# Performance work log

Hardware: AMD Instinct MI355X
Metric: run time of the kernel (lower is better)

Reference implementation:

```python
import jax, jax.numpy as jnp
import numpy as np
from jax import lax

B, C, H, W = 8, 128, 128, 128


def setup_inputs() -> dict:
    key = jax.random.key(0)
    ks = jax.random.split(key, 10)
    s = 0.02
    return {
        "x": jax.random.normal(ks[0], (B, C, H, W), jnp.float32),
        "ln_w": jnp.ones((C,), jnp.float32),
        "ln_b": jnp.zeros((C,), jnp.float32),
        "qkv_w": jax.random.normal(ks[1], (3 * C, C, 1, 1), jnp.float32) * s,
        "qkv_b": jnp.zeros((3 * C,), jnp.float32),
        "dw_w": jax.random.normal(ks[2], (3 * C, 1, 3, 3), jnp.float32) * s,
        "dw_b": jnp.zeros((3 * C,), jnp.float32),
        "proj_w": jax.random.normal(ks[3], (C, C, 1, 1), jnp.float32) * s,
        "proj_b": jnp.zeros((C,), jnp.float32),
        "temp1": jnp.ones((1, 1), jnp.float32),
        "temp2": jnp.ones((1, 1), jnp.float32),
    }


def reference(x, ln_w, ln_b, qkv_w, qkv_b, dw_w, dw_b, proj_w, proj_b, temp1, temp2):
    Cd = x.shape[1]

    def ln(t):  # WithBias LayerNorm over channel dim (unbiased=False var)
        mu = t.mean(axis=1, keepdims=True)
        var = ((t - mu) ** 2).mean(axis=1, keepdims=True)
        return (t - mu) / jnp.sqrt(var + 1e-5) * ln_w[None, :, None, None] + ln_b[None, :, None, None]

    def conv1(t, w, b):  # 1x1 conv
        return jnp.einsum('bchw,oc->bohw', t, w[:, :, 0, 0]) + b[None, :, None, None]

    def dwc(t):  # depthwise 3x3, pad 1
        y = lax.conv_general_dilated(t, dw_w, (1, 1), ((1, 1), (1, 1)),
                                     dimension_numbers=('NCHW', 'OIHW', 'NCHW'),
                                     feature_group_count=t.shape[1])
        return y + dw_b[None, :, None, None]

    def l2n(t):  # F.normalize over last axis, eps=1e-12
        return t / jnp.maximum(jnp.linalg.norm(t, axis=-1, keepdims=True), 1e-12)

    # ---- stage 1: pool over H, attention over W (channel-pooled) ----
    qkv = dwc(conv1(ln(x), qkv_w, qkv_b))
    q1, k1, v1 = qkv[:, :Cd], qkv[:, Cd:2 * Cd], qkv[:, 2 * Cd:]
    q1 = l2n(q1.mean(axis=2)[:, None])           # [B,1,C,W]
    k1 = l2n(k1.max(axis=2)[:, None])            # [B,1,C,W]
    attn1 = jax.nn.softmax(jnp.einsum('bocw,bocv->bowv', q1, k1) * temp1, axis=-1)  # [B,1,W,W]
    out1 = jnp.einsum('bchw,bowv->bchv', v1, attn1)
    out1 = x + conv1(out1, proj_w, proj_b)

    # ---- stage 2: pool over C, attention over H ----
    qkv = dwc(conv1(ln(out1), qkv_w, qkv_b))
    q2, k2, v2 = qkv[:, :Cd], qkv[:, Cd:2 * Cd], qkv[:, 2 * Cd:]
    q2 = l2n(q2.mean(axis=1)[:, None])           # [B,1,H,W]
    k2 = l2n(k2.mean(axis=1)[:, None])           # [B,1,H,W]
    attn2 = jax.nn.softmax(jnp.einsum('bohw,bogw->bohg', q2, k2) * temp2, axis=-1)  # [B,1,H,H]
    out2 = jnp.einsum('bchw,bohg->bcgw', v2, attn2)  # = (v^T @ attn)^T
    out = conv1(out2, proj_w, proj_b) + out1
    return out
```

## Files before the change

kernel.cpp:

```cpp
#include <hip/hip_runtime.h>

typedef __attribute__((ext_vector_type(8))) short bf16x8;
typedef __attribute__((ext_vector_type(4))) float f32x4;
typedef __attribute__((ext_vector_type(4))) unsigned short us4;
typedef __attribute__((ext_vector_type(4))) unsigned int u32x4;

static constexpr int CC = 128, NN = 16384;
static constexpr int O3 = 384;
static constexpr long long CN  = (long long)CC * NN;
static constexpr long long O3N = (long long)O3 * NN;

__device__ __forceinline__ float wave_sum(float v) {
  for (int o = 32; o; o >>= 1) v += __shfl_xor(v, o);
  return v;
}
__device__ __forceinline__ float wave_max(float v) {
  for (int o = 32; o; o >>= 1) v = fmaxf(v, __shfl_xor(v, o));
  return v;
}
__device__ __forceinline__ unsigned short f2bf(float f) {
  unsigned u = __float_as_uint(f);
  u += 0x7FFF + ((u >> 16) & 1);
  return (unsigned short)(u >> 16);
}
__device__ __forceinline__ float bf2f(unsigned short h) {
  return __uint_as_float((unsigned)h << 16);
}

__global__ __launch_bounds__(64) void k_prep(const float* __restrict__ qkvw,
                                             const float* __restrict__ qkvb,
                                             const float* __restrict__ lnw,
                                             const float* __restrict__ lnb,
                                             const float* __restrict__ projw,
                                             unsigned short* __restrict__ Aq,
                                             unsigned short* __restrict__ Ap,
                                             float* __restrict__ Svec,
                                             float* __restrict__ bias2) {
  int o = blockIdx.x, t = threadIdx.x;
  if (o < O3) {
    float w0 = qkvw[o * 128 + t], w1 = qkvw[o * 128 + t + 64];
    unsigned short h0 = f2bf(w0 * lnw[t]), h1 = f2bf(w1 * lnw[t + 64]);
    Aq[o * 128 + t] = h0; Aq[o * 128 + t + 64] = h1;
    float s = wave_sum(bf2f(h0) + bf2f(h1));
    float bs = wave_sum(w0 * lnb[t] + w1 * lnb[t + 64]);
    if (t == 0) { Svec[o] = s; bias2[o] = qkvb[o] + bs; }
  } else {
    int r = o - O3;
    Ap[r * 128 + t] = f2bf(projw[r * 128 + t]);
    Ap[r * 128 + t + 64] = f2bf(projw[r * 128 + t + 64]);
  }
}

__global__ __launch_bounds__(256) void k_qkv_mfma(
    const void* __restrict__ srcp, const float* __restrict__ mu, const float* __restrict__ rs,
    const unsigned short* __restrict__ Aq, const float* __restrict__ Svec,
    const float* __restrict__ bias2, unsigned short* __restrict__ out,
    int b0, int useg, int srcbf) {
  __shared__ unsigned short As[128 * 136];
  __shared__ unsigned short Bs[64 * 128];
  __shared__ float muL[64], rsL[64];
  int bz = blockIdx.z, bg = b0 + bz;
  int p = blockIdx.x;
  int hi = p / 24, rr0 = p - hi * 24;
  int m0 = (rr0 >> 3) * 128;
  int n0 = (hi * 8 + (rr0 & 7)) * 64;
  int t = threadIdx.x, w = t >> 6, l = t & 63;
  int lr = l & 15, lg = l >> 4;

  {
    const unsigned short* Asrc = Aq + (size_t)m0 * 128;
#pragma unroll
    for (int r = 0; r < 8; ++r) {
      int v = r * 256 + t;
      int m = v >> 4, c8 = (v & 15) * 8;
      *(u32x4*)&As[m * 136 + c8] = *(const u32x4*)&Asrc[m * 128 + c8];
    }
  }
  {
    int n = t & 63, cb = t >> 6;
    if (!srcbf) {
      const float* xb = (const float*)srcp + (size_t)bg * CN + n0;
      float xr[32];
#pragma unroll
      for (int g = 0; g < 4; ++g)
#pragma unroll
        for (int q = 0; q < 8; ++q)
          xr[g * 8 + q] = xb[(size_t)((cb * 4 + g) * 8 + q) * NN + n];
#pragma unroll
      for (int g = 0; g < 4; ++g) {
        int c8 = (cb * 4 + g) * 8;
        unsigned pk[4];
#pragma unroll
        for (int q = 0; q < 4; ++q) {
          unsigned short a = f2bf(xr[g * 8 + 2 * q]);
          unsigned short b = f2bf(xr[g * 8 + 2 * q + 1]);
          pk[q] = (unsigned)a | ((unsigned)b << 16);
        }
        int c8s = c8 ^ ((n & 7) << 3);
        *(u32x4*)&Bs[n * 128 + c8s] = *(const u32x4*)pk;
      }
    } else {
      const unsigned short* xb = (const unsigned short*)srcp + (size_t)bg * CN + n0;
      unsigned short xr[32];
#pragma unroll
      for (int g = 0; g < 4; ++g)
#pragma unroll
        for (int q = 0; q < 8; ++q)
          xr[g * 8 + q] = xb[(size_t)((cb * 4 + g) * 8 + q) * NN + n];
#pragma unroll
      for (int g = 0; g < 4; ++g) {
        int c8 = (cb * 4 + g) * 8;
        unsigned pk[4];
#pragma unroll
        for (int q = 0; q < 4; ++q)
          pk[q] = (unsigned)xr[g * 8 + 2 * q] | ((unsigned)xr[g * 8 + 2 * q + 1] << 16);
        int c8s = c8 ^ ((n & 7) << 3);
        *(u32x4*)&Bs[n * 128 + c8s] = *(const u32x4*)pk;
      }
    }
  }
  __syncthreads();

  if (!useg) {
    int pp = t >> 2, sub = t & 3;
    float s1 = 0.f, s2 = 0.f;
#pragma unroll
    for (int b2 = 0; b2 < 4; ++b2) {
      int c8 = (sub * 4 + b2) * 8;
      int c8s = c8 ^ ((pp & 7) << 3);
      bf16x8 v = *(const bf16x8*)&Bs[pp * 128 + c8s];
#pragma unroll
      for (int q = 0; q < 8; ++q) {
        float f = bf2f((unsigned short)v[q]);
        s1 += f; s2 += f * f;
      }
    }
    s1 += __shfl_xor(s1, 1); s2 += __shfl_xor(s2, 1);
    s1 += __shfl_xor(s1, 2); s2 += __shfl_xor(s2, 2);
    if (sub == 0) {
      float m = s1 * (1.f / 128.f);
      muL[pp] = m;
      rsL[pp] = rsqrtf(s2 * (1.f / 128.f) - m * m + 1e-5f);
    }
    __syncthreads();
  }

  f32x4 acc[2][4];
#pragma unroll
  for (int i = 0; i < 2; ++i)
#pragma unroll
    for (int j = 0; j < 4; ++j) acc[i][j] = (f32x4){0.f, 0.f, 0.f, 0.f};
#pragma unroll
  for (int ks = 0; ks < 4; ++ks) {
    bf16x8 bfr[4];
#pragma unroll
    for (int j = 0; j < 4; ++j) {
      int row = 16 * j + lr;
      int col = (ks * 32 + lg * 8) ^ ((lr & 7) << 3);
      bfr[j] = *(const bf16x8*)&Bs[row * 128 + col];
    }
#pragma unroll
    for (int i = 0; i < 2; ++i) {
      bf16x8 afr = *(const bf16x8*)&As[(32 * w + 16 * i + lr) * 136 + ks * 32 + lg * 8];
#pragma unroll
      for (int j = 0; j < 4; ++j)
        acc[i][j] = __builtin_amdgcn_mfma_f32_16x16x32_bf16(afr, bfr[j], acc[i][j], 0, 0, 0);
    }
  }

  float rsv[4], muv[4];
#pragma unroll
  for (int j = 0; j < 4; ++j) {
    int nl = 16 * j + lr;
    if (useg) {
      rsv[j] = rs[(size_t)bg * NN + n0 + nl];
      muv[j] = mu[(size_t)bg * NN + n0 + nl];
    } else {
      rsv[j] = rsL[nl];
      muv[j] = muL[nl];
    }
  }
  __syncthreads();
  unsigned short* Os = As;
#pragma unroll
  for (int i = 0; i < 2; ++i) {
    int obl = 32 * w + 16 * i + lg * 4;
    float sv[4], bv[4];
#pragma unroll
    for (int r2 = 0; r2 < 4; ++r2) { sv[r2] = Svec[m0 + obl + r2]; bv[r2] = bias2[m0 + obl + r2]; }
#pragma unroll
    for (int j = 0; j < 4; ++j)
#pragma unroll
      for (int r2 = 0; r2 < 4; ++r2)
        Os[(obl + r2) * 72 + 16 * j + lr] =
            f2bf(rsv[j] * (acc[i][j][r2] - muv[j] * sv[r2]) + bv[r2]);
  }
  __syncthreads();
#pragma unroll
  for (int r = 0; r < 4; ++r) {
    int idx = r * 256 + t;
    int row = idx >> 3, ch = idx & 7;
    unsigned short* op = out + (size_t)bz * O3N + (size_t)(m0 + row) * NN + n0 + ch * 8;
    *(u32x4*)op = *(const u32x4*)&Os[row * 72 + ch * 8];
  }
}

__global__ __launch_bounds__(1024) void k_dwc(unsigned short* __restrict__ buf,
                                              const float* __restrict__ dww,
                                              const float* __restrict__ dwb,
                                              float* __restrict__ qm,
                                              float* __restrict__ km,
                                              int b0, int stage) {
  __shared__ unsigned short pl[130 * 144];
  __shared__ float red[32 * 128];
  int o = blockIdx.x, bz = blockIdx.y, bg = b0 + bz;
  int t = threadIdx.x;
  unsigned short* base = buf + (size_t)bz * O3N + (size_t)o * NN;
  unsigned* pl32 = (unsigned*)pl;

  for (int i = t; i < 1168; i += 1024) {
    int idx;
    if (i < 72) idx = i;
    else if (i < 144) idx = 129 * 72 + (i - 72);
    else { int j = i - 144; int row = (j >> 3) + 1; int s = j & 7;
           idx = row * 72 + (s < 4 ? s : 64 + s); }
    pl32[idx] = 0u;
  }
  __syncthreads();
#pragma unroll
  for (int r = 0; r < 2; ++r) {
    int idx = r * 1024 + t;
    int row = idx >> 4, c8 = (idx & 15) * 8;
    *(u32x4*)&pl[(row + 1) * 144 + 8 + c8] = *(const u32x4*)&base[row * 128 + c8];
  }
  __syncthreads();

  const float* wg = dww + o * 9;
  float w00 = wg[0], w01 = wg[1], w02 = wg[2];
  float w10 = wg[3], w11 = wg[4], w12 = wg[5];
  float w20 = wg[6], w21 = wg[7], w22 = wg[8];
  float bias = dwb[o];
  int mode = (stage == 0) ? (o < 128 ? 1 : (o < 256 ? 2 : 0)) : 0;
  int hh0 = t >> 5, w0 = (t & 31) * 4;
  float csum[4] = {0.f, 0.f, 0.f, 0.f};
  float cmax[4] = {-1e30f, -1e30f, -1e30f, -1e30f};

#pragma unroll
  for (int g = 0; g < 4; ++g) {
    int h = g * 32 + hh0;
    float a0 = bias, a1 = bias, a2 = bias, a3 = bias;
#pragma unroll
    for (int dr = 0; dr < 3; ++dr) {
      const unsigned short* rp = &pl[(h + dr) * 144];
      us4 cA = *(const us4*)&rp[w0 + 4];
      us4 cB = *(const us4*)&rp[w0 + 8];
      us4 cC = *(const us4*)&rp[w0 + 12];
      float f0 = bf2f(cA[3]), f1 = bf2f(cB[0]), f2 = bf2f(cB[1]);
      float f3 = bf2f(cB[2]), f4 = bf2f(cB[3]), f5 = bf2f(cC[0]);
      float wr0 = (dr == 0) ? w00 : (dr == 1 ? w10 : w20);
      float wr1 = (dr == 0) ? w01 : (dr == 1 ? w11 : w21);
      float wr2 = (dr == 0) ? w02 : (dr == 1 ? w12 : w22);
      a0 += f0 * wr0 + f1 * wr1 + f2 * wr2;
      a1 += f1 * wr0 + f2 * wr1 + f3 * wr2;
      a2 += f2 * wr0 + f3 * wr1 + f4 * wr2;
      a3 += f3 * wr0 + f4 * wr1 + f5 * wr2;
    }
    if (mode == 0) {
      us4 ov;
      ov[0] = f2bf(a0); ov[1] = f2bf(a1); ov[2] = f2bf(a2); ov[3] = f2bf(a3);
      *(us4*)&base[g * 4096 + t * 4] = ov;
    } else if (mode == 1) {
      csum[0] += a0; csum[1] += a1; csum[2] += a2; csum[3] += a3;
    } else {
      cmax[0] = fmaxf(cmax[0], a0); cmax[1] = fmaxf(cmax[1], a1);
      cmax[2] = fmaxf(cmax[2], a2); cmax[3] = fmaxf(cmax[3], a3);
    }
  }

  if (mode) {
    int j = t >> 5;
#pragma unroll
    for (int dx = 0; dx < 4; ++dx)
      red[j * 128 + w0 + dx] = (mode == 1) ? csum[dx] : cmax[dx];
    __syncthreads();
    if (t < 128) {
      float v = red[t];
      if (mode == 1) {
        for (int jj = 1; jj < 32; ++jj) v += red[jj * 128 + t];
        qm[(size_t)bg * NN + o * 128 + t] = v * (1.f / 128.f);
      } else {
        for (int jj = 1; jj < 32; ++jj) v = fmaxf(v, red[jj * 128 + t]);
        km[(size_t)bg * NN + (o - 128) * 128 + t] = v;
      }
    }
  }
}

__global__ __launch_bounds__(256) void k_reduce2(const unsigned short* __restrict__ qkv,
                                                 float* __restrict__ qm, float* __restrict__ km,
                                                 int b0) {
  int bz = blockIdx.y;
  int n = blockIdx.x * 256 + threadIdx.x;
  const unsigned short* base = qkv + (size_t)bz * O3N + n;
  float sq = 0.f, sk = 0.f;
#pragma unroll 4
  for (int c = 0; c < 128; ++c) {
    sq += bf2f(base[(size_t)c * NN]);
    sk += bf2f(base[(size_t)(c + 128) * NN]);
  }
  size_t off = (size_t)(b0 + bz) * NN + n;
  qm[off] = sq * (1.f / 128.f);
  km[off] = sk * (1.f / 128.f);
}

__global__ void k_norm2(float* __restrict__ qm, float* __restrict__ km, int row0) {
  float* buf = blockIdx.y ? km : qm;
  int r = row0 + blockIdx.x, t = threadIdx.x;
  float* p = buf + (size_t)r * 128;
  float v0 = p[t], v1 = p[t + 64];
  float s = wave_sum(v0 * v0 + v1 * v1);
  float sc = 1.f / fmaxf(sqrtf(s), 1e-12f);
  p[t] = v0 * sc;
  p[t + 64] = v1 * sc;
}

__global__ void k_attn1(const float* __restrict__ qm, const float* __restrict__ km,
                        const float* __restrict__ temp, unsigned short* __restrict__ attnT,
                        int b0) {
  int bg = b0 + blockIdx.y;
  int i = blockIdx.x, t = threadIdx.x;
  const float* qb = qm + (size_t)bg * NN;
  const float* kb = km + (size_t)bg * NN;
  __shared__ float qcol[128];
  __shared__ float wred[2];
  qcol[t] = qb[t * 128 + i];
  __syncthreads();
  float s = 0.f;
#pragma unroll 4
  for (int k = 0; k < 128; ++k) s += qcol[k] * kb[k * 128 + t];
  s *= temp[0];
  int wid = t >> 6, lane = t & 63;
  float mx = wave_max(s);
  if (lane == 0) wred[wid] = mx;
  __syncthreads();
  mx = fmaxf(wred[0], wred[1]);
  float pv = __expf(s - mx);
  __syncthreads();
  float sm = wave_sum(pv);
  if (lane == 0) wred[wid] = sm;
  __syncthreads();
  float denom = wred[0] + wred[1];
  attnT[(size_t)bg * NN + (size_t)t * 128 + i] = f2bf(pv / denom);
}

__global__ void k_attn2(const float* __restrict__ qm, const float* __restrict__ km,
                        const float* __restrict__ temp, unsigned short* __restrict__ attnT,
                        int b0) {
  int bg = b0 + blockIdx.y;
  int i = blockIdx.x, t = threadIdx.x;
  const float* qb = qm + (size_t)bg * NN + i * 128;
  const float* kb = km + (size_t)bg * NN + (size_t)t * 128;
  __shared__ float qrow[128];
  __shared__ float wred[2];
  qrow[t] = qb[t];
  __syncthreads();
  float s = 0.f;
#pragma unroll 4
  for (int w = 0; w < 128; ++w) s += qrow[w] * kb[w];
  s *= temp[0];
  int wid = t >> 6, lane = t & 63;
  float mx = wave_max(s);
  if (lane == 0) wred[wid] = mx;
  __syncthreads();
  mx = fmaxf(wred[0], wred[1]);
  float pv = __expf(s - mx);
  __syncthreads();
  float sm = wave_sum(pv);
  if (lane == 0) wred[wid] = sm;
  __syncthreads();
  float denom = wred[0] + wred[1];
  attnT[(size_t)bg * NN + (size_t)t * 128 + i] = f2bf(pv / denom);
}

__global__ __launch_bounds__(256) void k_ap1(const unsigned short* __restrict__ buf,
                                             const unsigned short* __restrict__ attnT,
                                             const unsigned short* __restrict__ Ap,
                                             const float* __restrict__ pb,
                                             const float* __restrict__ x,
                                             unsigned short* __restrict__ out1,
                                             float* __restrict__ mu, float* __restrict__ rs,
                                             int b0) {
  __shared__ __attribute__((aligned(16))) unsigned short S[32768];
  unsigned short* TA = S;
  unsigned short* TB = S + 16384;
  int h = blockIdx.x, bz = blockIdx.z, bg = b0 + bz;
  int t = threadIdx.x, wv = t >> 6, l = t & 63, lr = l & 15, lg = l >> 4;

  {
    const unsigned short* vbase = buf + (size_t)bz * O3N + (size_t)256 * NN;
    const unsigned short* abase = attnT + (size_t)bg * NN;
#pragma unroll
    for (int r = 0; r < 8; ++r) {
      int idx = r * 256 + t;
      int row = idx >> 4, c8 = (idx & 15) * 8;
      int c8s = c8 ^ ((row & 7) << 3);
      *(u32x4*)&TA[row * 128 + c8s] = *(const u32x4*)&vbase[((size_t)row * 128 + h) * 128 + c8];
      *(u32x4*)&TB[row * 128 + c8s] = *(const u32x4*)&abase[row * 128 + c8];
    }
  }
  __syncthreads();

  f32x4 acc[2][8];
#pragma unroll
  for (int i = 0; i < 2; ++i)
#pragma unroll
    for (int j = 0; j < 8; ++j) acc[i][j] = (f32x4){0.f, 0.f, 0.f, 0.f};
#pragma unroll
  for (int ks = 0; ks < 4; ++ks) {
    int colx = (ks * 32 + lg * 8) ^ ((lr & 7) << 3);
    bf16x8 bfr[8];
#pragma unroll
    for (int j = 0; j < 8; ++j)
      bfr[j] = *(const bf16x8*)&TB[(16 * j + lr) * 128 + colx];
#pragma unroll
    for (int i = 0; i < 2; ++i) {
      bf16x8 afr = *(const bf16x8*)&TA[(32 * wv + 16 * i + lr) * 128 + colx];
#pragma unroll
      for (int j = 0; j < 8; ++j)
        acc[i][j] = __builtin_amdgcn_mfma_f32_16x16x32_bf16(afr, bfr[j], acc[i][j], 0, 0, 0);
    }
  }
  __syncthreads();

#pragma unroll
  for (int i = 0; i < 2; ++i) {
    int c0 = 32 * wv + 16 * i + lg * 4;
#pragma unroll
    for (int j = 0; j < 8; ++j) {
      int v = 16 * j + lr;
      us4 ov;
#pragma unroll
      for (int r2 = 0; r2 < 4; ++r2) ov[r2] = f2bf(acc[i][j][r2]);
      *(us4*)&TA[v * 128 + (c0 ^ ((v & 7) << 3))] = ov;
    }
  }
#pragma unroll
  for (int r = 0; r < 8; ++r) {
    int idx = r * 256 + t;
    int row = idx >> 4, c8 = (idx & 15) * 8;
    *(u32x4*)&TB[row * 128 + (c8 ^ ((row & 7) << 3))] = *(const u32x4*)&Ap[row * 128 + c8];
  }
  __syncthreads();

#pragma unroll
  for (int i = 0; i < 2; ++i)
#pragma unroll
    for (int j = 0; j < 8; ++j) acc[i][j] = (f32x4){0.f, 0.f, 0.f, 0.f};
#pragma unroll
  for (int ks = 0; ks < 4; ++ks) {
    int colx = (ks * 32 + lg * 8) ^ ((lr & 7) << 3);
    bf16x8 bfr[8];
#pragma unroll
    for (int j = 0; j < 8; ++j)
      bfr[j] = *(const bf16x8*)&TA[(16 * j + lr) * 128 + colx];
#pragma unroll
    for (int i = 0; i < 2; ++i) {
      bf16x8 afr = *(const bf16x8*)&TB[(32 * wv + 16 * i + lr) * 128 + colx];
#pragma unroll
      for (int j = 0; j < 8; ++j)
        acc[i][j] = __builtin_amdgcn_mfma_f32_16x16x32_bf16(afr, bfr[j], acc[i][j], 0, 0, 0);
    }
  }
  __syncthreads();

  unsigned short* Os = S;
  float* red1 = (float*)(S + 17408);
  float* red2 = red1 + 128 * 17;
  float s1p[8], s2p[8];
#pragma unroll
  for (int j = 0; j < 8; ++j) { s1p[j] = 0.f; s2p[j] = 0.f; }
#pragma unroll
  for (int i = 0; i < 2; ++i) {
    int o0 = 32 * wv + 16 * i + lg * 4;
    float bv[4];
#pragma unroll
    for (int r2 = 0; r2 < 4; ++r2) bv[r2] = pb[o0 + r2];
#pragma unroll
    for (int j = 0; j < 8; ++j) {
      int n = h * 128 + 16 * j + lr;
#pragma unroll
      for (int r2 = 0; r2 < 4; ++r2) {
        size_t off = (size_t)bg * CN + (size_t)(o0 + r2) * NN + n;
        float val = acc[i][j][r2] + bv[r2] + x[off];
        Os[(o0 + r2) * 136 + 16 * j + lr] = f2bf(val);
        s1p[j] += val;
        s2p[j] += val * val;
      }
    }
  }
#pragma unroll
  for (int j = 0; j < 8; ++j) {
    red1[(16 * j + lr) * 17 + (wv * 4 + lg)] = s1p[j];
    red2[(16 * j + lr) * 17 + (wv * 4 + lg)] = s2p[j];
  }
  __syncthreads();
#pragma unroll
  for (int r = 0; r < 8; ++r) {
    int idx = r * 256 + t;
    int row = idx >> 4, ch = idx & 15;
    unsigned short* op = out1 + (size_t)bg * CN + (size_t)row * NN + h * 128 + ch * 8;
    *(u32x4*)op = *(const u32x4*)&Os[row * 136 + ch * 8];
  }
  if (t < 128) {
    float s1 = 0.f, s2 = 0.f;
#pragma unroll
    for (int kk = 0; kk < 16; ++kk) { s1 += red1[t * 17 + kk]; s2 += red2[t * 17 + kk]; }
    float m = s1 * (1.f / 128.f);
    float var = s2 * (1.f / 128.f) - m * m;
    mu[(size_t)bg * NN + h * 128 + t] = m;
    rs[(size_t)bg * NN + h * 128 + t] = rsqrtf(var + 1e-5f);
  }
}

__global__ __launch_bounds__(256) void k_apply2_mfma(unsigned short* __restrict__ buf,
                                                     const unsigned short* __restrict__ attnT,
                                                     int b0) {
  __shared__ unsigned short At[128 * 136];
  __shared__ unsigned short Bt[128 * 136];
  int bz = blockIdx.z, bg = b0 + bz, c = blockIdx.x;
  int t = threadIdx.x, w = t >> 6, l = t & 63, lr = l & 15, lg = l >> 4;
  const unsigned short* vsrc = buf + (size_t)bz * O3N + (size_t)(256 + c) * NN;
  const unsigned short* asrc = attnT + (size_t)bg * NN;
#pragma unroll
  for (int r = 0; r < 8; ++r) {
    int idx = r * 256 + t;
    int row = idx >> 4, c8 = (idx & 15) * 8;
    *(u32x4*)&At[row * 136 + c8] = *(const u32x4*)&asrc[row * 128 + c8];
    us4 lo = *(const us4*)&vsrc[row * 128 + c8];
    us4 hi = *(const us4*)&vsrc[row * 128 + c8 + 4];
#pragma unroll
    for (int q = 0; q < 4; ++q) {
      Bt[(c8 + q) * 136 + row] = lo[q];
      Bt[(c8 + 4 + q) * 136 + row] = hi[q];
    }
  }
  __syncthreads();
  f32x4 acc[2][8];
#pragma unroll
  for (int i = 0; i < 2; ++i)
#pragma unroll
    for (int j = 0; j < 8; ++j) acc[i][j] = (f32x4){0.f, 0.f, 0.f, 0.f};
#pragma unroll
  for (int ks = 0; ks < 4; ++ks) {
    bf16x8 bfr[8];
#pragma unroll
    for (int j = 0; j < 8; ++j)
      bfr[j] = *(const bf16x8*)&Bt[(16 * j + lr) * 136 + ks * 32 + lg * 8];
#pragma unroll
    for (int i = 0; i < 2; ++i) {
      bf16x8 afr = *(const bf16x8*)&At[(32 * w + 16 * i + lr) * 136 + ks * 32 + lg * 8];
#pragma unroll
      for (int j = 0; j < 8; ++j)
        acc[i][j] = __builtin_amdgcn_mfma_f32_16x16x32_bf16(afr, bfr[j], acc[i][j], 0, 0, 0);
    }
  }
  __syncthreads();
  unsigned short* Os = At;
#pragma unroll
  for (int i = 0; i < 2; ++i)
#pragma unroll
    for (int j = 0; j < 8; ++j)
#pragma unroll
      for (int r2 = 0; r2 < 4; ++r2) {
        int g = 32 * w + 16 * i + lg * 4 + r2;
        Os[g * 136 + 16 * j + lr] = f2bf(acc[i][j][r2]);
      }
  __syncthreads();
  unsigned short* ob = buf + (size_t)bz * O3N + (size_t)c * NN;
#pragma unroll
  for (int r = 0; r < 8; ++r) {
    int idx = r * 256 + t;
    int row = idx >> 4, ch = idx & 15;
    *(u32x4*)&ob[(size_t)row * 128 + ch * 8] = *(const u32x4*)&Os[row * 136 + ch * 8];
  }
}

__global__ __launch_bounds__(256) void k_proj_mfma(
    const unsigned short* __restrict__ tin, const unsigned short* __restrict__ Ap,
    const float* __restrict__ pb, const unsigned short* __restrict__ res,
    float* __restrict__ dst, int b0) {
  __shared__ unsigned short Al[128 * 136];
  __shared__ unsigned short Bs2[64 * 128];
  int bz = blockIdx.z, bg = b0 + bz;
  int n0 = blockIdx.x * 64;
  int t = threadIdx.x, w = t >> 6, l = t & 63, lr = l & 15, lg = l >> 4;
  const unsigned short* tb = tin + (size_t)bz * O3N + n0;

#pragma unroll
  for (int r = 0; r < 8; ++r) {
    int v = r * 256 + t;
    int m = v >> 4, c8 = (v & 15) * 8;
    *(u32x4*)&Al[m * 136 + c8] = *(const u32x4*)&Ap[m * 128 + c8];
  }
  {
    int n = t & 63, cb = t >> 6;
    unsigned short vr[32];
#pragma unroll
    for (int g = 0; g < 4; ++g)
#pragma unroll
      for (int q = 0; q < 8; ++q)
        vr[g * 8 + q] = tb[(size_t)((cb * 4 + g) * 8 + q) * NN + n];
#pragma unroll
    for (int g = 0; g < 4; ++g) {
      int c8 = (cb * 4 + g) * 8;
      unsigned pk[4];
#pragma unroll
      for (int q = 0; q < 4; ++q)
        pk[q] = (unsigned)vr[g * 8 + 2 * q] | ((unsigned)vr[g * 8 + 2 * q + 1] << 16);
      int c8s = c8 ^ ((n & 7) << 3);
      *(u32x4*)&Bs2[n * 128 + c8s] = *(const u32x4*)pk;
    }
  }
  __syncthreads();

  f32x4 acc[2][4];
#pragma unroll
  for (int i = 0; i < 2; ++i)
#pragma unroll
    for (int j = 0; j < 4; ++j) acc[i][j] = (f32x4){0.f, 0.f, 0.f, 0.f};

#pragma unroll
  for (int ks = 0; ks < 4; ++ks) {
    bf16x8 bfr[4];
#pragma unroll
    for (int j = 0; j < 4; ++j) {
      int row = 16 * j + lr;
      int col = (ks * 32 + lg * 8) ^ ((lr & 7) << 3);
      bfr[j] = *(const bf16x8*)&Bs2[row * 128 + col];
    }
#pragma unroll
    for (int i = 0; i < 2; ++i) {
      bf16x8 afr = *(const bf16x8*)&Al[(32 * w + 16 * i + lr) * 136 + ks * 32 + lg * 8];
#pragma unroll
      for (int j = 0; j < 4; ++j)
        acc[i][j] = __builtin_amdgcn_mfma_f32_16x16x32_bf16(afr, bfr[j], acc[i][j], 0, 0, 0);
    }
  }

#pragma unroll
  for (int i = 0; i < 2; ++i) {
    int ob = 32 * w + 16 * i + lg * 4;
    float bv[4];
#pragma unroll
    for (int r2 = 0; r2 < 4; ++r2) bv[r2] = pb[ob + r2];
#pragma unroll
    for (int j = 0; j < 4; ++j) {
      int n = n0 + 16 * j + lr;
#pragma unroll
      for (int r2 = 0; r2 < 4; ++r2) {
        size_t off = (size_t)bg * CN + (size_t)(ob + r2) * NN + n;
        dst[off] = acc[i][j][r2] + bv[r2] + bf2f(res[off]);
      }
    }
  }
}

extern "C" void kernel_launch(void* const* d_in, const int* in_sizes, int n_in,
                              void* d_out, int out_size, void* d_ws, size_t ws_size,
                              hipStream_t stream) {
  (void)in_sizes; (void)n_in; (void)out_size;
  const float* x     = (const float*)d_in[0];
  const float* lnw   = (const float*)d_in[1];
  const float* lnb   = (const float*)d_in[2];
  const float* qkvw  = (const float*)d_in[3];
  const float* qkvb  = (const float*)d_in[4];
  const float* dww   = (const float*)d_in[5];
  const float* dwb   = (const float*)d_in[6];
  const float* projw = (const float*)d_in[7];
  const float* projb = (const float*)d_in[8];
  const float* temp1 = (const float*)d_in[9];
  const float* temp2 = (const float*)d_in[10];
  float* out = (float*)d_out;
  float* ws = (float*)d_ws;

  auto needBytes = [&](int nb) {
    return ((size_t)nb * (O3N / 2) + 4ull * CN + 4ull * 131072 + 65536 + 768 + 24576 + 8192) * 4;
  };
  int NB = 8;
  while (NB > 1 && ws_size < needBytes(NB)) NB >>= 1;
  if (ws_size < needBytes(1)) return;

  unsigned short* convbuf = (unsigned short*)ws;
  unsigned short* out1 = (unsigned short*)(ws + (size_t)NB * (O3N / 2));
  float* mu = ws + (size_t)NB * (O3N / 2) + 4ull * CN;
  float* rs = mu + 131072;
  float* qm = rs + 131072;
  float* km = qm + 131072;
  unsigned short* attnT = (unsigned short*)(km + 131072);
  float* Svec  = (float*)(attnT + 8ull * NN);
  float* bias2 = Svec + 384;
  unsigned short* Aq = (unsigned short*)(bias2 + 384);
  unsigned short* Ap = Aq + 49152;

  k_prep<<<512, 64, 0, stream>>>(qkvw, qkvb, lnw, lnb, projw, Aq, Ap, Svec, bias2);

  for (int b0 = 0; b0 < 8; b0 += NB) {
    k_qkv_mfma<<<dim3(768, 1, NB), 256, 0, stream>>>(x, mu, rs, Aq, Svec, bias2, convbuf,
                                                     b0, 0, 0);
    k_dwc<<<dim3(384, NB), 1024, 0, stream>>>(convbuf, dww, dwb, qm, km, b0, 0);
    k_norm2<<<dim3(NB * 128, 2), 64, 0, stream>>>(qm, km, b0 * 128);
    k_attn1<<<dim3(128, NB), 128, 0, stream>>>(qm, km, temp1, attnT, b0);
    k_ap1<<<dim3(128, 1, NB), 256, 0, stream>>>(convbuf, attnT, Ap, projb, x, out1, mu, rs, b0);
  }
  for (int b0 = 0; b0 < 8; b0 += NB) {
    k_qkv_mfma<<<dim3(768, 1, NB), 256, 0, stream>>>(out1, mu, rs, Aq, Svec, bias2, convbuf,
                                                     b0, 1, 1);
    k_dwc<<<dim3(384, NB), 1024, 0, stream>>>(convbuf, dww, dwb, qm, km, b0, 1);
    k_reduce2<<<dim3(64, NB), 256, 0, stream>>>(convbuf, qm, km, b0);
    k_norm2<<<dim3(NB * 128, 2), 64, 0, stream>>>(qm, km, b0 * 128);
    k_attn2<<<dim3(128, NB), 128, 0, stream>>>(qm, km, temp2, attnT, b0);
    k_apply2_mfma<<<dim3(128, 1, NB), 256, 0, stream>>>(convbuf, attnT, b0);
    k_proj_mfma<<<dim3(256, 1, NB), 256, 0, stream>>>(convbuf, Ap, projb, out1, out, b0);
  }
}
```

Baseline: 276.3 us.

## Vectorize B-tile global loads, use packed bf16 conversions, merge syncs

After: 276.8 us. No clear change (+0.2%).

```diff
diff --git a/kernel.cpp b/kernel.cpp
--- a/kernel.cpp
+++ b/kernel.cpp
@@ -1,4 +1,5 @@
 #include <hip/hip_runtime.h>
+#include <hip/hip_bf16.h>
 
 typedef __attribute__((ext_vector_type(8))) short bf16x8;
 typedef __attribute__((ext_vector_type(4))) float f32x4;
@@ -14,14 +15,13 @@
   for (int o = 32; o; o >>= 1) v += __shfl_xor(v, o);
   return v;
 }
-__device__ __forceinline__ float wave_max(float v) {
-  for (int o = 32; o; o >>= 1) v = fmaxf(v, __shfl_xor(v, o));
-  return v;
+__device__ __forceinline__ unsigned pk2bf(float a, float b) {
+  __hip_bfloat162 h = __float22bfloat162_rn(make_float2(a, b));
+  return *reinterpret_cast<unsigned*>(&h);
 }
 __device__ __forceinline__ unsigned short f2bf(float f) {
-  unsigned u = __float_as_uint(f);
-  u += 0x7FFF + ((u >> 16) & 1);
-  return (unsigned short)(u >> 16);
+  __hip_bfloat16 h = __float2bfloat16(f);
+  return *reinterpret_cast<unsigned short*>(&h);
 }
 __device__ __forceinline__ float bf2f(unsigned short h) {
   return __uint_as_float((unsigned)h << 16);
@@ -77,45 +77,37 @@
     }
   }
   {
-    int n = t & 63, cb = t >> 6;
+    int pg = t & 15, cbk = t >> 4;
+    int c8 = cbk * 8;
     if (!srcbf) {
-      const float* xb = (const float*)srcp + (size_t)bg * CN + n0;
-      float xr[32];
-#pragma unroll
-      for (int g = 0; g < 4; ++g)
-#pragma unroll
-        for (int q = 0; q < 8; ++q)
-          xr[g * 8 + q] = xb[(size_t)((cb * 4 + g) * 8 + q) * NN + n];
-#pragma unroll
-      for (int g = 0; g < 4; ++g) {
-        int c8 = (cb * 4 + g) * 8;
+      const float* xb = (const float*)srcp + (size_t)bg * CN + n0 + pg * 4;
+      float4 v[8];
+#pragma unroll
+      for (int ch = 0; ch < 8; ++ch)
+        v[ch] = *(const float4*)&xb[(size_t)(c8 + ch) * NN];
+#pragma unroll
+      for (int pp = 0; pp < 4; ++pp) {
         unsigned pk[4];
 #pragma unroll
-        for (int q = 0; q < 4; ++q) {
-          unsigned short a = f2bf(xr[g * 8 + 2 * q]);
-          unsigned short b = f2bf(xr[g * 8 + 2 * q + 1]);
-          pk[q] = (unsigned)a | ((unsigned)b << 16);
-        }
-        int c8s = c8 ^ ((n & 7) << 3);
-        *(u32x4*)&Bs[n * 128 + c8s] = *(const u32x4*)pk;
+        for (int q = 0; q < 4; ++q)
+          pk[q] = pk2bf(((const float*)&v[2 * q])[pp], ((const float*)&v[2 * q + 1])[pp]);
+        int n = pg * 4 + pp;
+        *(u32x4*)&Bs[n * 128 + (c8 ^ ((n & 7) << 3))] = *(const u32x4*)pk;
       }
     } else {
-      const unsigned short* xb = (const unsigned short*)srcp + (size_t)bg * CN + n0;
-      unsigned short xr[32];
-#pragma unroll
-      for (int g = 0; g < 4; ++g)
-#pragma unroll
-        for (int q = 0; q < 8; ++q)
-          xr[g * 8 + q] = xb[(size_t)((cb * 4 + g) * 8 + q) * NN + n];
-#pragma unroll
-      for (int g = 0; g < 4; ++g) {
-        int c8 = (cb * 4 + g) * 8;
+      const unsigned short* xb = (const unsigned short*)srcp + (size_t)bg * CN + n0 + pg * 4;
+      us4 v[8];
+#pragma unroll
+      for (int ch = 0; ch < 8; ++ch)
+        v[ch] = *(const us4*)&xb[(size_t)(c8 + ch) * NN];
+#pragma unroll
+      for (int pp = 0; pp < 4; ++pp) {
         unsigned pk[4];
 #pragma unroll
         for (int q = 0; q < 4; ++q)
-          pk[q] = (unsigned)xr[g * 8 + 2 * q] | ((unsigned)xr[g * 8 + 2 * q + 1] << 16);
-        int c8s = c8 ^ ((n & 7) << 3);
-        *(u32x4*)&Bs[n * 128 + c8s] = *(const u32x4*)pk;
+          pk[q] = (unsigned)v[2 * q][pp] | ((unsigned)v[2 * q + 1][pp] << 16);
+        int n = pg * 4 + pp;
+        *(u32x4*)&Bs[n * 128 + (c8 ^ ((n & 7) << 3))] = *(const u32x4*)pk;
       }
     }
   }
@@ -142,7 +134,6 @@
       muL[pp] = m;
       rsL[pp] = rsqrtf(s2 * (1.f / 128.f) - m * m + 1e-5f);
     }
-    __syncthreads();
   }
 
   f32x4 acc[2][4];
@@ -167,6 +158,7 @@
         acc[i][j] = __builtin_amdgcn_mfma_f32_16x16x32_bf16(afr, bfr[j], acc[i][j], 0, 0, 0);
     }
   }
+  __syncthreads();
 
   float rsv[4], muv[4];
 #pragma unroll
@@ -180,7 +172,6 @@
       muv[j] = muL[nl];
     }
   }
-  __syncthreads();
   unsigned short* Os = As;
 #pragma unroll
   for (int i = 0; i < 2; ++i) {
@@ -189,11 +180,13 @@
 #pragma unroll
     for (int r2 = 0; r2 < 4; ++r2) { sv[r2] = Svec[m0 + obl + r2]; bv[r2] = bias2[m0 + obl + r2]; }
 #pragma unroll
-    for (int j = 0; j < 4; ++j)
+    for (int j = 0; j < 4; ++j) {
+      float rm = rsv[j] * muv[j];
 #pragma unroll
       for (int r2 = 0; r2 < 4; ++r2)
         Os[(obl + r2) * 72 + 16 * j + lr] =
-            f2bf(rsv[j] * (acc[i][j][r2] - muv[j] * sv[r2]) + bv[r2]);
+            f2bf(fmaf(rsv[j], acc[i][j][r2], bv[r2] - rm * sv[r2]));
+    }
   }
   __syncthreads();
 #pragma unroll
@@ -266,9 +259,9 @@
       a3 += f3 * wr0 + f4 * wr1 + f5 * wr2;
     }
     if (mode == 0) {
-      us4 ov;
-      ov[0] = f2bf(a0); ov[1] = f2bf(a1); ov[2] = f2bf(a2); ov[3] = f2bf(a3);
-      *(us4*)&base[g * 4096 + t * 4] = ov;
+      unsigned lo = pk2bf(a0, a1), hi2 = pk2bf(a2, a3);
+      uint2 ov = make_uint2(lo, hi2);
+      *(uint2*)&base[g * 4096 + t * 4] = ov;
     } else if (mode == 1) {
       csum[0] += a0; csum[1] += a1; csum[2] += a2; csum[3] += a3;
     } else {
@@ -333,6 +326,7 @@
   const float* kb = km + (size_t)bg * NN;
   __shared__ float qcol[128];
   __shared__ float wred[2];
+  float mxw, smw;
   qcol[t] = qb[t * 128 + i];
   __syncthreads();
   float s = 0.f;
@@ -340,14 +334,15 @@
   for (int k = 0; k < 128; ++k) s += qcol[k] * kb[k * 128 + t];
   s *= temp[0];
   int wid = t >> 6, lane = t & 63;
-  float mx = wave_max(s);
-  if (lane == 0) wred[wid] = mx;
-  __syncthreads();
-  mx = fmaxf(wred[0], wred[1]);
+  mxw = s;
+  for (int o = 32; o; o >>= 1) mxw = fmaxf(mxw, __shfl_xor(mxw, o));
+  if (lane == 0) wred[wid] = mxw;
+  __syncthreads();
+  float mx = fmaxf(wred[0], wred[1]);
   float pv = __expf(s - mx);
   __syncthreads();
-  float sm = wave_sum(pv);
-  if (lane == 0) wred[wid] = sm;
+  smw = wave_sum(pv);
+  if (lane == 0) wred[wid] = smw;
   __syncthreads();
   float denom = wred[0] + wred[1];
   attnT[(size_t)bg * NN + (size_t)t * 128 + i] = f2bf(pv / denom);
@@ -369,14 +364,15 @@
   for (int w = 0; w < 128; ++w) s += qrow[w] * kb[w];
   s *= temp[0];
   int wid = t >> 6, lane = t & 63;
-  float mx = wave_max(s);
-  if (lane == 0) wred[wid] = mx;
-  __syncthreads();
-  mx = fmaxf(wred[0], wred[1]);
+  float mxw = s;
+  for (int o = 32; o; o >>= 1) mxw = fmaxf(mxw, __shfl_xor(mxw, o));
+  if (lane == 0) wred[wid] = mxw;
+  __syncthreads();
+  float mx = fmaxf(wred[0], wred[1]);
   float pv = __expf(s - mx);
   __syncthreads();
-  float sm = wave_sum(pv);
-  if (lane == 0) wred[wid] = sm;
+  float smw = wave_sum(pv);
+  if (lane == 0) wred[wid] = smw;
   __syncthreads();
   float denom = wred[0] + wred[1];
   attnT[(size_t)bg * NN + (size_t)t * 128 + i] = f2bf(pv / denom);
@@ -438,10 +434,9 @@
 #pragma unroll
     for (int j = 0; j < 8; ++j) {
       int v = 16 * j + lr;
-      us4 ov;
-#pragma unroll
-      for (int r2 = 0; r2 < 4; ++r2) ov[r2] = f2bf(acc[i][j][r2]);
-      *(us4*)&TA[v * 128 + (c0 ^ ((v & 7) << 3))] = ov;
+      uint2 ov = make_uint2(pk2bf(acc[i][j][0], acc[i][j][1]),
+                            pk2bf(acc[i][j][2], acc[i][j][3]));
+      *(uint2*)&TA[v * 128 + (c0 ^ ((v & 7) << 3))] = ov;
     }
   }
 #pragma unroll
@@ -569,12 +564,13 @@
 #pragma unroll
   for (int i = 0; i < 2; ++i)
 #pragma unroll
-    for (int j = 0; j < 8; ++j)
-#pragma unroll
-      for (int r2 = 0; r2 < 4; ++r2) {
-        int g = 32 * w + 16 * i + lg * 4 + r2;
-        Os[g * 136 + 16 * j + lr] = f2bf(acc[i][j][r2]);
-      }
+    for (int j = 0; j < 8; ++j) {
+      int g = 32 * w + 16 * i + lg * 4;
+      Os[g * 136 + 16 * j + lr + 0 * 136] = f2bf(acc[i][j][0]);
+      Os[(g + 1) * 136 + 16 * j + lr] = f2bf(acc[i][j][1]);
+      Os[(g + 2) * 136 + 16 * j + lr] = f2bf(acc[i][j][2]);
+      Os[(g + 3) * 136 + 16 * j + lr] = f2bf(acc[i][j][3]);
+    }
   __syncthreads();
   unsigned short* ob = buf + (size_t)bz * O3N + (size_t)c * NN;
 #pragma unroll
@@ -594,7 +590,6 @@
   int bz = blockIdx.z, bg = b0 + bz;
   int n0 = blockIdx.x * 64;
   int t = threadIdx.x, w = t >> 6, l = t & 63, lr = l & 15, lg = l >> 4;
-  const unsigned short* tb = tin + (size_t)bz * O3N + n0;
 
 #pragma unroll
   for (int r = 0; r < 8; ++r) {
@@ -603,22 +598,21 @@
     *(u32x4*)&Al[m * 136 + c8] = *(const u32x4*)&Ap[m * 128 + c8];
   }
   {
-    int n = t & 63, cb = t >> 6;
-    unsigned short vr[32];
-#pragma unroll
-    for (int g = 0; g < 4; ++g)
-#pragma unroll
-      for (int q = 0; q < 8; ++q)
-        vr[g * 8 + q] = tb[(size_t)((cb * 4 + g) * 8 + q) * NN + n];
-#pragma unroll
-    for (int g = 0; g < 4; ++g) {
-      int c8 = (cb * 4 + g) * 8;
+    int pg = t & 15, cbk = t >> 4;
+    int c8 = cbk * 8;
+    const unsigned short* tb = tin + (size_t)bz * O3N + n0 + pg * 4;
+    us4 v[8];
+#pragma unroll
+    for (int ch = 0; ch < 8; ++ch)
+      v[ch] = *(const us4*)&tb[(size_t)(c8 + ch) * NN];
+#pragma unroll
+    for (int pp = 0; pp < 4; ++pp) {
       unsigned pk[4];
 #pragma unroll
       for (int q = 0; q < 4; ++q)
-        pk[q] = (unsigned)vr[g * 8 + 2 * q] | ((unsigned)vr[g * 8 + 2 * q + 1] << 16);
-      int c8s = c8 ^ ((n & 7) << 3);
-      *(u32x4*)&Bs2[n * 128 + c8s] = *(const u32x4*)pk;
+        pk[q] = (unsigned)v[2 * q][pp] | ((unsigned)v[2 * q + 1][pp] << 16);
+      int n = pg * 4 + pp;
+      *(u32x4*)&Bs2[n * 128 + (c8 ^ ((n & 7) << 3))] = *(const u32x4*)pk;
     }
   }
   __syncthreads();
```
